# Kernel optimization log

Measured on AMD Instinct MI355X. Metric: run time of the kernel, lower is better.

## Reference

```python
import jax, jax.numpy as jnp
import numpy as np

D_EEG = 256; D_QUERY = 256; D_MODEL = 256; NUM_HEADS = 8
D_HEAD = D_MODEL // NUM_HEADS; PROJ_DIM = 40
B = 32; N = 4096


def _rope(x):
    # x: (B, S, H, D) -- rotate along sequence dim with interleaved-pair convention
    S, D = x.shape[1], x.shape[-1]
    inv = 1.0 / (10000.0 ** (jnp.arange(0, D, 2, dtype=jnp.float32) / D))
    f = jnp.arange(S, dtype=jnp.float32)[:, None] * inv[None, :]        # (S, D/2)
    cos = jnp.repeat(jnp.cos(f), 2, axis=-1)[None, :, None, :]
    sin = jnp.repeat(jnp.sin(f), 2, axis=-1)[None, :, None, :]
    xp = x.reshape(x.shape[:-1] + (D // 2, 2))
    rot = jnp.stack([-xp[..., 1], xp[..., 0]], axis=-1).reshape(x.shape)
    return x * cos + rot * sin


def _ln(x, g, b):
    m = x.mean(-1, keepdims=True)
    v = x.var(-1, keepdims=True)
    return (x - m) / jnp.sqrt(v + 1e-5) * g + b


def _l2norm(x):
    return x / jnp.maximum(jnp.linalg.norm(x, axis=-1, keepdims=True), 1e-12)


def setup_inputs():
    key = jax.random.key(0)
    ks = jax.random.split(key, 16)

    def lin(k, din, dout):
        s = 1.0 / np.sqrt(din)
        w = jax.random.uniform(k, (din, dout), minval=-s, maxval=s, dtype=jnp.float32)
        b = jax.random.uniform(jax.random.fold_in(k, 1), (dout,), minval=-s, maxval=s, dtype=jnp.float32)
        return w, b

    eeg_w, eeg_b = lin(ks[0], D_EEG, D_MODEL)
    stim_w, stim_b = lin(ks[1], D_QUERY, D_MODEL)
    temp_w, temp_b = lin(ks[2], D_QUERY, D_MODEL)
    q_w, q_b = lin(ks[3], D_MODEL, D_MODEL)
    k_w, k_b = lin(ks[4], D_MODEL, D_MODEL)
    v_w, v_b = lin(ks[5], D_MODEL, D_MODEL)
    fc_w, fc_b = lin(ks[6], D_MODEL, PROJ_DIM)

    return {
        "eeg_feat": jax.random.normal(ks[7], (B, N, D_EEG), dtype=jnp.float32),
        "stim_feat": jax.random.normal(ks[8], (B, D_QUERY), dtype=jnp.float32),
        "temp_feat": jax.random.normal(ks[9], (B, D_QUERY), dtype=jnp.float32),
        "eeg_w": eeg_w, "eeg_b": eeg_b,
        "stim_w": stim_w, "stim_b": stim_b,
        "temp_w": temp_w, "temp_b": temp_b,
        "q_w": q_w, "q_b": q_b,
        "k_w": k_w, "k_b": k_b,
        "v_w": v_w, "v_b": v_b,
        "fc_w": fc_w, "fc_b": fc_b,
        "lnq_g": jnp.ones((D_MODEL,), jnp.float32), "lnq_b": jnp.zeros((D_MODEL,), jnp.float32),
        "lnk_g": jnp.ones((D_MODEL,), jnp.float32), "lnk_b": jnp.zeros((D_MODEL,), jnp.float32),
    }


def reference(eeg_feat, stim_feat, temp_feat, eeg_w, eeg_b, stim_w, stim_b,
              temp_w, temp_b, q_w, q_b, k_w, k_b, v_w, v_b, fc_w, fc_b,
              lnq_g, lnq_b, lnk_g, lnk_b):
    Bq = eeg_feat.shape[0]
    eeg = eeg_feat @ eeg_w + eeg_b                      # (B, N, D)
    stim = (stim_feat @ stim_w + stim_b)[:, None, :]
    temp = (temp_feat @ temp_w + temp_b)[:, None, :]
    query = jnp.concatenate([stim, temp], axis=1)        # (B, 2, D)

    query = _ln(query, lnq_g, lnq_b)
    kv = _ln(eeg, lnk_g, lnk_b)

    Q = (query @ q_w + q_b).reshape(Bq, 2, NUM_HEADS, D_HEAD)
    K = (kv @ k_w + k_b).reshape(Bq, -1, NUM_HEADS, D_HEAD)
    V = (kv @ v_w + v_b).reshape(Bq, -1, NUM_HEADS, D_HEAD)

    Q = _l2norm(_rope(Q))
    K = _l2norm(_rope(K))

    scores = jnp.einsum('bqhd,bkhd->bhqk', Q, K) / np.sqrt(D_HEAD)
    scale = jax.lax.stop_gradient(
        jnp.maximum(jnp.std(scores, axis=-1, ddof=1, keepdims=True), 1e-3))
    scores = jnp.tanh(scores / (2.0 * scale)) * (5.0 * scale)

    w = jax.nn.softmax(scores, axis=-1)
    w = (w + 1e-4) / (w.sum(-1, keepdims=True) + 1e-8)

    attn_out = jnp.einsum('bhqk,bkhd->bqhd', w, V).reshape(Bq, 2, D_MODEL)
    pooled = attn_out.mean(axis=1)
    logits = pooled @ fc_w + fc_b
    return logits, pooled, attn_out, query
```

## Files before the change

### kernel.cpp

```cpp
#include <hip/hip_runtime.h>
#include <hip/hip_bf16.h>
#include <math.h>

#define TID ((int)threadIdx.x)

typedef float f32x4 __attribute__((ext_vector_type(4)));
typedef short s16x8 __attribute__((ext_vector_type(8)));

__device__ __forceinline__ unsigned short f2bf(float f) {
  union { float f; unsigned u; } v; v.f = f;
  unsigned r = v.u + 0x7FFFu + ((v.u >> 16) & 1u);
  return (unsigned short)(r >> 16);
}
__device__ __forceinline__ float bf2f(unsigned short h) {
  union { unsigned u; float f; } v; v.u = ((unsigned)h) << 16;
  return v.f;
}

__global__ void prep_kernel(const float* __restrict__ eeg_w,
                            const float* __restrict__ k_w,
                            const float* __restrict__ v_w,
                            unsigned short* __restrict__ wt,
                            float2* __restrict__ trig) {
  int gid = blockIdx.x * 256 + TID;
  if (gid < 3 * 65536) {
    int m = gid >> 16, e = gid & 65535;
    int i = e >> 8, j = e & 255;
    const float* W = (m == 0) ? eeg_w : ((m == 1) ? k_w : v_w);
    wt[m * 65536 + j * 256 + i] = f2bf(W[i * 256 + j]);
  } else {
    int e = gid - 3 * 65536;
    int n = e >> 4, p = e & 15;
    float inv = exp2f(-(float)p * 0.8304820237218406f);
    float a = (float)n * inv;
    trig[e] = make_float2(cosf(a), sinf(a));
  }
}

__global__ __launch_bounds__(256) void q_kernel(
    const float* __restrict__ stim_feat, const float* __restrict__ temp_feat,
    const float* __restrict__ stim_w, const float* __restrict__ stim_b,
    const float* __restrict__ temp_w, const float* __restrict__ temp_b,
    const float* __restrict__ q_w, const float* __restrict__ q_b,
    const float* __restrict__ lnq_g, const float* __restrict__ lnq_b,
    float* __restrict__ out_query, float* __restrict__ qhat) {
  int b = blockIdx.x >> 1, q = blockIdx.x & 1;
  __shared__ float f[256];
  __shared__ float red[8];
  const float* feat = (q ? temp_feat : stim_feat) + b * 256;
  const float* W = q ? temp_w : stim_w;
  const float* bias = q ? temp_b : stim_b;
  f[TID] = feat[TID];
  __syncthreads();
  float acc = bias[TID];
#pragma unroll 8
  for (int i = 0; i < 256; ++i) acc = fmaf(f[i], W[i * 256 + TID], acc);
  float s1 = acc, s2 = acc * acc;
#pragma unroll
  for (int m = 1; m < 64; m <<= 1) { s1 += __shfl_xor(s1, m, 64); s2 += __shfl_xor(s2, m, 64); }
  if ((TID & 63) == 0) { red[TID >> 6] = s1; red[4 + (TID >> 6)] = s2; }
  __syncthreads();
  s1 = red[0] + red[1] + red[2] + red[3];
  s2 = red[4] + red[5] + red[6] + red[7];
  float mean = s1 * (1.f / 256.f);
  float var = s2 * (1.f / 256.f) - mean * mean;
  float rstd = rsqrtf(var + 1e-5f);
  float qln = (acc - mean) * rstd * lnq_g[TID] + lnq_b[TID];
  out_query[(b * 2 + q) * 256 + TID] = qln;
  __syncthreads();
  f[TID] = qln;
  __syncthreads();
  float a2 = q_b[TID];
#pragma unroll 8
  for (int i = 0; i < 256; ++i) a2 = fmaf(f[i], q_w[i * 256 + TID], a2);
  __syncthreads();
  f[TID] = a2;
  __syncthreads();
  float partner = f[TID ^ 1];
  int p = (TID >> 1) & 15;
  float inv = exp2f(-(float)p * 0.8304820237218406f);
  float ang = (float)q * inv;
  float cc_ = cosf(ang), ss_ = sinf(ang);
  float r = (TID & 1) ? fmaf(a2, cc_, partner * ss_) : fmaf(a2, cc_, -partner * ss_);
  float sq = r * r;
#pragma unroll
  for (int m = 1; m < 32; m <<= 1) sq += __shfl_xor(sq, m, 32);
  float rs = 1.f / fmaxf(sqrtf(sq), 1e-12f);
  qhat[(b * 2 + q) * 256 + TID] = r * rs;
}

__global__ __launch_bounds__(256) void main_kernel(
    const float* __restrict__ x,
    const float* __restrict__ eeg_b,
    const float* __restrict__ k_b,
    const float* __restrict__ v_b,
    const float* __restrict__ lnk_g,
    const float* __restrict__ lnk_b,
    const unsigned short* __restrict__ wt_eeg,
    const unsigned short* __restrict__ wt_k,
    const unsigned short* __restrict__ wt_v,
    const float2* __restrict__ trig,
    const float* __restrict__ qhat,
    float* __restrict__ scores,
    unsigned short* __restrict__ vws) {

  __shared__ __align__(16) unsigned short A[64 * 256];
  __shared__ __align__(16) unsigned short K2[64 * 256];
  __shared__ __align__(16) float TRQH[2048];
  __shared__ float2 ST[64];

  float* PS = (float*)K2;
  float2* TR = (float2*)TRQH;

  const int tid = TID;
  const int w = tid >> 6, l = tid & 63, g = l >> 4, c = l & 15;
  const int r0 = blockIdx.x * 64;
  const int b = r0 >> 12;
  const int n0 = r0 & 4095;

#pragma unroll
  for (int i = 0; i < 8; ++i) {
    int ch = i * 256 + tid;
    int row = ch >> 5, cc = ch & 31;
    const float4* gp = (const float4*)(x + (size_t)(r0 + row) * 256 + cc * 8);
    float4 u0 = gp[0], u1 = gp[1];
    s16x8 pk;
    pk[0] = (short)f2bf(u0.x); pk[1] = (short)f2bf(u0.y);
    pk[2] = (short)f2bf(u0.z); pk[3] = (short)f2bf(u0.w);
    pk[4] = (short)f2bf(u1.x); pk[5] = (short)f2bf(u1.y);
    pk[6] = (short)f2bf(u1.z); pk[7] = (short)f2bf(u1.w);
    *(s16x8*)&A[row * 256 + ((cc ^ (row & 7)) * 8)] = pk;
  }
#pragma unroll
  for (int i = 0; i < 4; ++i) {
    int e = i * 256 + tid;
    int rr = e >> 4, pp = e & 15;
    TR[e] = trig[(size_t)(n0 + rr) * 16 + pp];
  }
  __syncthreads();

  f32x4 acc[4][4];

#define DO_GEMM(WT) do {                                                          \
    _Pragma("unroll") for (int rb = 0; rb < 4; ++rb)                              \
      _Pragma("unroll") for (int cb = 0; cb < 4; ++cb)                            \
        acc[rb][cb] = (f32x4){0.f, 0.f, 0.f, 0.f};                                \
    _Pragma("unroll") for (int ks = 0; ks < 8; ++ks) {                            \
      s16x8 af[4]; s16x8 bfr[4];                                                  \
      _Pragma("unroll") for (int rb = 0; rb < 4; ++rb) {                          \
        int row = rb * 16 + c; int kc = ks * 4 + g;                               \
        af[rb] = *(const s16x8*)&A[row * 256 + ((kc ^ (row & 7)) * 8)];           \
      }                                                                           \
      _Pragma("unroll") for (int cb = 0; cb < 4; ++cb) {                          \
        int col = w * 64 + cb * 16 + c;                                           \
        bfr[cb] = *(const s16x8*)&(WT)[col * 256 + ks * 32 + g * 8];              \
      }                                                                           \
      _Pragma("unroll") for (int rb = 0; rb < 4; ++rb)                            \
        _Pragma("unroll") for (int cb = 0; cb < 4; ++cb)                          \
          acc[rb][cb] = __builtin_amdgcn_mfma_f32_16x16x32_bf16(                  \
              af[rb], bfr[cb], acc[rb][cb], 0, 0, 0);                             \
    } } while (0)

  float ebias[4], kbias[4], vbias[4], gg[4], bb[4];
  int cols[4];
#pragma unroll
  for (int cb = 0; cb < 4; ++cb) {
    int col = w * 64 + cb * 16 + c;
    cols[cb] = col;
    ebias[cb] = eeg_b[col]; kbias[cb] = k_b[col]; vbias[cb] = v_b[col];
    gg[cb] = lnk_g[col]; bb[cb] = lnk_b[col];
  }

  DO_GEMM(wt_eeg);

  {
    float ps[4][4], pq[4][4];
#pragma unroll
    for (int rb = 0; rb < 4; ++rb)
#pragma unroll
      for (int r = 0; r < 4; ++r) {
        float s = 0.f, q2 = 0.f;
#pragma unroll
        for (int cb = 0; cb < 4; ++cb) {
          float v = acc[rb][cb][r] + ebias[cb];
          s += v; q2 += v * v;
        }
        ps[rb][r] = s; pq[rb][r] = q2;
      }
#pragma unroll
    for (int m = 1; m < 16; m <<= 1)
#pragma unroll
      for (int rb = 0; rb < 4; ++rb)
#pragma unroll
        for (int r = 0; r < 4; ++r) {
          ps[rb][r] += __shfl_xor(ps[rb][r], m, 64);
          pq[rb][r] += __shfl_xor(pq[rb][r], m, 64);
        }
    float outS = 0.f, outQ = 0.f;
#pragma unroll
    for (int rb = 0; rb < 4; ++rb)
#pragma unroll
      for (int r = 0; r < 4; ++r)
        if (c == rb * 4 + r) { outS = ps[rb][r]; outQ = pq[rb][r]; }
    int row = (c >> 2) * 16 + g * 4 + (c & 3);
    PS[row * 8 + w * 2 + 0] = outS;
    PS[row * 8 + w * 2 + 1] = outQ;
  }
  __syncthreads();
  if (tid < 64) {
    float s = PS[tid * 8 + 0] + PS[tid * 8 + 2] + PS[tid * 8 + 4] + PS[tid * 8 + 6];
    float q2 = PS[tid * 8 + 1] + PS[tid * 8 + 3] + PS[tid * 8 + 5] + PS[tid * 8 + 7];
    float mean = s * (1.f / 256.f);
    float var = q2 * (1.f / 256.f) - mean * mean;
    ST[tid] = make_float2(mean, rsqrtf(var + 1e-5f));
  }
  __syncthreads();

#pragma unroll
  for (int rb = 0; rb < 4; ++rb)
#pragma unroll
    for (int r = 0; r < 4; ++r) {
      int row = rb * 16 + g * 4 + r;
      float2 st = ST[row];
#pragma unroll
      for (int cb = 0; cb < 4; ++cb) {
        float v = (acc[rb][cb][r] + ebias[cb] - st.x) * st.y * gg[cb] + bb[cb];
        A[row * 256 + (cols[cb] ^ ((row & 7) * 8))] = f2bf(v);
      }
    }
  __syncthreads();

  DO_GEMM(wt_k);
#pragma unroll
  for (int rb = 0; rb < 4; ++rb)
#pragma unroll
    for (int cb = 0; cb < 4; ++cb) {
      int pp = (cols[cb] >> 1) & 15;
#pragma unroll
      for (int r = 0; r < 4; ++r) {
        int row = rb * 16 + g * 4 + r;
        float v = acc[rb][cb][r] + kbias[cb];
        float pv = __shfl_xor(v, 1, 64);
        float2 cs2 = TR[row * 16 + pp];
        float rv = (c & 1) ? fmaf(v, cs2.x, pv * cs2.y)
                           : fmaf(v, cs2.x, -pv * cs2.y);
        K2[row * 256 + (cols[cb] ^ ((row & 7) * 8))] = f2bf(rv);
      }
    }

  DO_GEMM(wt_v);
  __syncthreads();

#pragma unroll
  for (int rb = 0; rb < 4; ++rb)
#pragma unroll
    for (int r = 0; r < 4; ++r) {
      int row = rb * 16 + g * 4 + r;
#pragma unroll
      for (int cb = 0; cb < 4; ++cb)
        A[row * 256 + cols[cb]] = f2bf(acc[rb][cb][r] + vbias[cb]);
    }
  TRQH[tid] = qhat[(size_t)b * 512 + tid];
  TRQH[256 + tid] = qhat[(size_t)b * 512 + 256 + tid];
  __syncthreads();

#pragma unroll
  for (int i = 0; i < 2; ++i) {
    int hr = i * 256 + tid;
    int row = hr >> 3, hh = hr & 7;
    const s16x8* src = (const s16x8*)&A[row * 256 + hh * 32];
    s16x8 v0 = src[0], v1 = src[1], v2 = src[2], v3 = src[3];
    s16x8* dst = (s16x8*)&vws[((size_t)(b * 8 + hh) * 4096 + n0 + row) * 32];
    dst[0] = v0; dst[1] = v1; dst[2] = v2; dst[3] = v3;
  }

#pragma unroll
  for (int cell = 0; cell < 2; ++cell) {
    int h = cell * 4 + w;
    int row = l;
    float ssq = 0.f, d0 = 0.f, d1 = 0.f;
#pragma unroll
    for (int j = 0; j < 4; ++j) {
      s16x8 kv = *(const s16x8*)&K2[row * 256 + (((h * 4 + j) ^ (row & 7)) * 8)];
#pragma unroll
      for (int t = 0; t < 8; ++t) {
        float kf = bf2f((unsigned short)kv[t]);
        int col = h * 32 + j * 8 + t;
        ssq = fmaf(kf, kf, ssq);
        d0 = fmaf(kf, TRQH[col], d0);
        d1 = fmaf(kf, TRQH[256 + col], d1);
      }
    }
    float is = 0.17677669529663687f / fmaxf(sqrtf(ssq), 1e-12f);
    scores[(size_t)((b * 8 + h) * 2 + 0) * 4096 + n0 + row] = d0 * is;
    scores[(size_t)((b * 8 + h) * 2 + 1) * 4096 + n0 + row] = d1 * is;
  }
#undef DO_GEMM
}

__global__ __launch_bounds__(256) void attn_kernel(
    const float* __restrict__ scores,
    const unsigned short* __restrict__ vws,
    float* __restrict__ out_attn) {
  int b = blockIdx.x >> 3, h = blockIdx.x & 7;
  const float* s0p = scores + (size_t)((b * 8 + h) * 2 + 0) * 4096;
  const float* s1p = scores + (size_t)((b * 8 + h) * 2 + 1) * 4096;
  float sa[16], sb[16];
  float a1 = 0.f, a2 = 0.f, b1 = 0.f, b2 = 0.f;
#pragma unroll
  for (int i = 0; i < 16; ++i) {
    int k = i * 256 + TID;
    sa[i] = s0p[k]; sb[i] = s1p[k];
    a1 += sa[i]; a2 += sa[i] * sa[i];
    b1 += sb[i]; b2 += sb[i] * sb[i];
  }
  __shared__ float red[16];
  int w = TID >> 6;
#pragma unroll
  for (int m = 1; m < 64; m <<= 1) {
    a1 += __shfl_xor(a1, m, 64); a2 += __shfl_xor(a2, m, 64);
    b1 += __shfl_xor(b1, m, 64); b2 += __shfl_xor(b2, m, 64);
  }
  if ((TID & 63) == 0) { red[w * 4] = a1; red[w * 4 + 1] = a2; red[w * 4 + 2] = b1; red[w * 4 + 3] = b2; }
  __syncthreads();
  a1 = red[0] + red[4] + red[8] + red[12];
  a2 = red[1] + red[5] + red[9] + red[13];
  b1 = red[2] + red[6] + red[10] + red[14];
  b2 = red[3] + red[7] + red[11] + red[15];
  float va = (a2 - a1 * a1 * (1.f / 4096.f)) * (1.f / 4095.f);
  float vb = (b2 - b1 * b1 * (1.f / 4096.f)) * (1.f / 4095.f);
  float sga = fmaxf(sqrtf(fmaxf(va, 0.f)), 1e-3f);
  float sgb = fmaxf(sqrtf(fmaxf(vb, 0.f)), 1e-3f);
  float ia = 0.5f / sga, ib = 0.5f / sgb;
  float fa = 5.f * sga, fb = 5.f * sgb;
  float ea = 0.f, eb = 0.f;
#pragma unroll
  for (int i = 0; i < 16; ++i) {
    sa[i] = __expf(tanhf(sa[i] * ia) * fa);
    sb[i] = __expf(tanhf(sb[i] * ib) * fb);
    ea += sa[i]; eb += sb[i];
  }
#pragma unroll
  for (int m = 1; m < 64; m <<= 1) { ea += __shfl_xor(ea, m, 64); eb += __shfl_xor(eb, m, 64); }
  __syncthreads();
  if ((TID & 63) == 0) { red[w * 2] = ea; red[w * 2 + 1] = eb; }
  __syncthreads();
  ea = red[0] + red[2] + red[4] + red[6];
  eb = red[1] + red[3] + red[5] + red[7];
  float iea = 1.f / ea, ieb = 1.f / eb;
  float oa[32], ob[32];
#pragma unroll
  for (int d = 0; d < 32; ++d) { oa[d] = 0.f; ob[d] = 0.f; }
  const unsigned short* vbase = vws + (size_t)(b * 8 + h) * 4096 * 32;
#pragma unroll 4
  for (int i = 0; i < 16; ++i) {
    int k = i * 256 + TID;
    float wa = fmaf(sa[i], iea, 1e-4f);
    float wb = fmaf(sb[i], ieb, 1e-4f);
    const s16x8* vp = (const s16x8*)(vbase + (size_t)k * 32);
#pragma unroll
    for (int j = 0; j < 4; ++j) {
      s16x8 vv = vp[j];
#pragma unroll
      for (int t = 0; t < 8; ++t) {
        float vf = bf2f((unsigned short)vv[t]);
        oa[j * 8 + t] = fmaf(wa, vf, oa[j * 8 + t]);
        ob[j * 8 + t] = fmaf(wb, vf, ob[j * 8 + t]);
      }
    }
  }
#pragma unroll
  for (int m = 1; m < 64; m <<= 1) {
#pragma unroll
    for (int d = 0; d < 32; ++d) { oa[d] += __shfl_xor(oa[d], m, 64); ob[d] += __shfl_xor(ob[d], m, 64); }
  }
  __shared__ float R[4][64];
  if ((TID & 63) == 0) {
#pragma unroll
    for (int d = 0; d < 32; ++d) { R[w][d] = oa[d]; R[w][32 + d] = ob[d]; }
  }
  __syncthreads();
  if (TID < 64) {
    float s = R[0][TID] + R[1][TID] + R[2][TID] + R[3][TID];
    int q = TID >> 5, d = TID & 31;
    out_attn[(b * 2 + q) * 256 + h * 32 + d] = s;
  }
}

__global__ __launch_bounds__(256) void final_kernel(
    const float* __restrict__ attn, const float* __restrict__ fc_w,
    const float* __restrict__ fc_b, float* __restrict__ out_pooled,
    float* __restrict__ out_logits) {
  int b = blockIdx.x;
  __shared__ float P[256];
  float p = 0.5f * (attn[(b * 2) * 256 + TID] + attn[(b * 2 + 1) * 256 + TID]);
  out_pooled[b * 256 + TID] = p;
  P[TID] = p;
  __syncthreads();
  if (TID < 40) {
    float acc = fc_b[TID];
#pragma unroll 8
    for (int i = 0; i < 256; ++i) acc = fmaf(P[i], fc_w[i * 40 + TID], acc);
    out_logits[b * 40 + TID] = acc;
  }
}

extern "C" void kernel_launch(void* const* d_in, const int* in_sizes, int n_in,
                              void* d_out, int out_size, void* d_ws, size_t ws_size,
                              hipStream_t stream) {
  (void)in_sizes; (void)n_in; (void)out_size; (void)ws_size;
  const float* eeg_feat  = (const float*)d_in[0];
  const float* stim_feat = (const float*)d_in[1];
  const float* temp_feat = (const float*)d_in[2];
  const float* eeg_w = (const float*)d_in[3];
  const float* eeg_b = (const float*)d_in[4];
  const float* stim_w = (const float*)d_in[5];
  const float* stim_b = (const float*)d_in[6];
  const float* temp_w = (const float*)d_in[7];
  const float* temp_b = (const float*)d_in[8];
  const float* q_w = (const float*)d_in[9];
  const float* q_b = (const float*)d_in[10];
  const float* k_w = (const float*)d_in[11];
  const float* k_b = (const float*)d_in[12];
  const float* v_w = (const float*)d_in[13];
  const float* v_b = (const float*)d_in[14];
  const float* fc_w = (const float*)d_in[15];
  const float* fc_b = (const float*)d_in[16];
  const float* lnq_g = (const float*)d_in[17];
  const float* lnq_b = (const float*)d_in[18];
  const float* lnk_g = (const float*)d_in[19];
  const float* lnk_b = (const float*)d_in[20];

  char* ws = (char*)d_ws;
  unsigned short* wt  = (unsigned short*)(ws + 0);
  float2* trig        = (float2*)(ws + 393216);
  float* qhat         = (float*)(ws + 917504);
  float* scores       = (float*)(ws + 1048576);
  unsigned short* vws = (unsigned short*)(ws + 9437184);

  float* out = (float*)d_out;
  float* out_logits = out;
  float* out_pooled = out + 1280;
  float* out_attn   = out + 9472;
  float* out_query  = out + 25856;

  prep_kernel<<<1024, 256, 0, stream>>>(eeg_w, k_w, v_w, wt, trig);
  q_kernel<<<64, 256, 0, stream>>>(stim_feat, temp_feat, stim_w, stim_b,
                                   temp_w, temp_b, q_w, q_b, lnq_g, lnq_b,
                                   out_query, qhat);
  main_kernel<<<2048, 256, 0, stream>>>(eeg_feat, eeg_b, k_b, v_b, lnk_g, lnk_b,
                                        wt, wt + 65536, wt + 131072,
                                        trig, qhat, scores, vws);
  attn_kernel<<<256, 256, 0, stream>>>(scores, vws, out_attn);
  final_kernel<<<32, 256, 0, stream>>>(out_attn, fc_w, fc_b, out_pooled, out_logits);
}
```

Measured before the change: 255.5 us.

## Split fused main kernel into LN-projection and K/V kernels with register-cached weights

The single fused kernel is split into two. The first does the eeg projection and LayerNorm, preloads the weight fragments into registers, and writes the normalized bf16 activations to a workspace buffer. The second uses 512-thread blocks where half the waves compute K and half compute V concurrently, loops over four 64-row tiles per block, and prefetches the next tile from global memory into registers. This aims to reduce register pressure and raise occupancy and parallelism, at the cost of an extra 64 MB bf16 round trip through global memory and an additional kernel launch.

```diff
diff --git a/kernel.cpp b/kernel.cpp
--- a/kernel.cpp
+++ b/kernel.cpp
@@ -16,6 +16,9 @@
   union { unsigned u; float f; } v; v.u = ((unsigned)h) << 16;
   return v.f;
 }
+
+#define BAR_LGKM() do { asm volatile("s_waitcnt lgkmcnt(0)" ::: "memory"); \
+                        __builtin_amdgcn_s_barrier(); } while (0)
 
 __global__ void prep_kernel(const float* __restrict__ eeg_w,
                             const float* __restrict__ k_w,
@@ -89,34 +92,28 @@
   qhat[(b * 2 + q) * 256 + TID] = r * rs;
 }
 
-__global__ __launch_bounds__(256) void main_kernel(
+__global__ __launch_bounds__(256, 2) void eeg_ln_kernel(
     const float* __restrict__ x,
     const float* __restrict__ eeg_b,
-    const float* __restrict__ k_b,
-    const float* __restrict__ v_b,
     const float* __restrict__ lnk_g,
     const float* __restrict__ lnk_b,
     const unsigned short* __restrict__ wt_eeg,
-    const unsigned short* __restrict__ wt_k,
-    const unsigned short* __restrict__ wt_v,
-    const float2* __restrict__ trig,
-    const float* __restrict__ qhat,
-    float* __restrict__ scores,
-    unsigned short* __restrict__ vws) {
+    unsigned short* __restrict__ xp) {
 
   __shared__ __align__(16) unsigned short A[64 * 256];
-  __shared__ __align__(16) unsigned short K2[64 * 256];
-  __shared__ __align__(16) float TRQH[2048];
+  __shared__ float PS[64 * 8];
   __shared__ float2 ST[64];
-
-  float* PS = (float*)K2;
-  float2* TR = (float2*)TRQH;
 
   const int tid = TID;
   const int w = tid >> 6, l = tid & 63, g = l >> 4, c = l & 15;
   const int r0 = blockIdx.x * 64;
-  const int b = r0 >> 12;
-  const int n0 = r0 & 4095;
+
+  s16x8 bA[8][2];
+#pragma unroll
+  for (int ks = 0; ks < 8; ++ks)
+#pragma unroll
+    for (int j = 0; j < 2; ++j)
+      bA[ks][j] = *(const s16x8*)&wt_eeg[(size_t)(w * 64 + j * 16 + c) * 256 + ks * 32 + g * 8];
 
 #pragma unroll
   for (int i = 0; i < 8; ++i) {
@@ -131,47 +128,57 @@
     pk[6] = (short)f2bf(u1.z); pk[7] = (short)f2bf(u1.w);
     *(s16x8*)&A[row * 256 + ((cc ^ (row & 7)) * 8)] = pk;
   }
-#pragma unroll
-  for (int i = 0; i < 4; ++i) {
-    int e = i * 256 + tid;
-    int rr = e >> 4, pp = e & 15;
-    TR[e] = trig[(size_t)(n0 + rr) * 16 + pp];
-  }
-  __syncthreads();
-
-  f32x4 acc[4][4];
-
-#define DO_GEMM(WT) do {                                                          \
-    _Pragma("unroll") for (int rb = 0; rb < 4; ++rb)                              \
-      _Pragma("unroll") for (int cb = 0; cb < 4; ++cb)                            \
-        acc[rb][cb] = (f32x4){0.f, 0.f, 0.f, 0.f};                                \
-    _Pragma("unroll") for (int ks = 0; ks < 8; ++ks) {                            \
-      s16x8 af[4]; s16x8 bfr[4];                                                  \
-      _Pragma("unroll") for (int rb = 0; rb < 4; ++rb) {                          \
-        int row = rb * 16 + c; int kc = ks * 4 + g;                               \
-        af[rb] = *(const s16x8*)&A[row * 256 + ((kc ^ (row & 7)) * 8)];           \
-      }                                                                           \
-      _Pragma("unroll") for (int cb = 0; cb < 4; ++cb) {                          \
-        int col = w * 64 + cb * 16 + c;                                           \
-        bfr[cb] = *(const s16x8*)&(WT)[col * 256 + ks * 32 + g * 8];              \
-      }                                                                           \
-      _Pragma("unroll") for (int rb = 0; rb < 4; ++rb)                            \
-        _Pragma("unroll") for (int cb = 0; cb < 4; ++cb)                          \
-          acc[rb][cb] = __builtin_amdgcn_mfma_f32_16x16x32_bf16(                  \
-              af[rb], bfr[cb], acc[rb][cb], 0, 0, 0);                             \
-    } } while (0)
-
-  float ebias[4], kbias[4], vbias[4], gg[4], bb[4];
+
+  float ebias[4], gg[4], bb[4];
   int cols[4];
 #pragma unroll
   for (int cb = 0; cb < 4; ++cb) {
     int col = w * 64 + cb * 16 + c;
     cols[cb] = col;
-    ebias[cb] = eeg_b[col]; kbias[cb] = k_b[col]; vbias[cb] = v_b[col];
-    gg[cb] = lnk_g[col]; bb[cb] = lnk_b[col];
-  }
-
-  DO_GEMM(wt_eeg);
+    ebias[cb] = eeg_b[col]; gg[cb] = lnk_g[col]; bb[cb] = lnk_b[col];
+  }
+  __syncthreads();
+
+  f32x4 acc[4][4];
+#pragma unroll
+  for (int rb = 0; rb < 4; ++rb)
+#pragma unroll
+    for (int cb = 0; cb < 4; ++cb) acc[rb][cb] = (f32x4){0.f, 0.f, 0.f, 0.f};
+
+#pragma unroll
+  for (int ks = 0; ks < 8; ++ks) {
+    s16x8 af[4];
+#pragma unroll
+    for (int rb = 0; rb < 4; ++rb) {
+      int row = rb * 16 + c; int kc = ks * 4 + g;
+      af[rb] = *(const s16x8*)&A[row * 256 + ((kc ^ (row & 7)) * 8)];
+    }
+#pragma unroll
+    for (int rb = 0; rb < 4; ++rb)
+#pragma unroll
+      for (int j = 0; j < 2; ++j)
+        acc[rb][j] = __builtin_amdgcn_mfma_f32_16x16x32_bf16(af[rb], bA[ks][j], acc[rb][j], 0, 0, 0);
+  }
+  s16x8 bB[8][2];
+#pragma unroll
+  for (int ks = 0; ks < 8; ++ks)
+#pragma unroll
+    for (int j = 0; j < 2; ++j)
+      bB[ks][j] = *(const s16x8*)&wt_eeg[(size_t)(w * 64 + (2 + j) * 16 + c) * 256 + ks * 32 + g * 8];
+#pragma unroll
+  for (int ks = 0; ks < 8; ++ks) {
+    s16x8 af[4];
+#pragma unroll
+    for (int rb = 0; rb < 4; ++rb) {
+      int row = rb * 16 + c; int kc = ks * 4 + g;
+      af[rb] = *(const s16x8*)&A[row * 256 + ((kc ^ (row & 7)) * 8)];
+    }
+#pragma unroll
+    for (int rb = 0; rb < 4; ++rb)
+#pragma unroll
+      for (int j = 0; j < 2; ++j)
+        acc[rb][2 + j] = __builtin_amdgcn_mfma_f32_16x16x32_bf16(af[rb], bB[ks][j], acc[rb][2 + j], 0, 0, 0);
+  }
 
   {
     float ps[4][4], pq[4][4];
@@ -230,72 +237,166 @@
     }
   __syncthreads();
 
-  DO_GEMM(wt_k);
-#pragma unroll
-  for (int rb = 0; rb < 4; ++rb)
-#pragma unroll
-    for (int cb = 0; cb < 4; ++cb) {
-      int pp = (cols[cb] >> 1) & 15;
-#pragma unroll
-      for (int r = 0; r < 4; ++r) {
-        int row = rb * 16 + g * 4 + r;
-        float v = acc[rb][cb][r] + kbias[cb];
-        float pv = __shfl_xor(v, 1, 64);
-        float2 cs2 = TR[row * 16 + pp];
-        float rv = (c & 1) ? fmaf(v, cs2.x, pv * cs2.y)
-                           : fmaf(v, cs2.x, -pv * cs2.y);
-        K2[row * 256 + (cols[cb] ^ ((row & 7) * 8))] = f2bf(rv);
+#pragma unroll
+  for (int j = 0; j < 8; ++j) {
+    int gidx = tid + 256 * j;
+    *(s16x8*)&xp[(size_t)r0 * 256 + (size_t)gidx * 8] = *(const s16x8*)&A[gidx * 8];
+  }
+}
+
+__global__ __launch_bounds__(512, 2) void kv_kernel(
+    const unsigned short* __restrict__ xp,
+    const float* __restrict__ k_b,
+    const float* __restrict__ v_b,
+    const unsigned short* __restrict__ wt_k,
+    const unsigned short* __restrict__ wt_v,
+    const float2* __restrict__ trig,
+    const float* __restrict__ qhat,
+    float* __restrict__ scores,
+    unsigned short* __restrict__ vws) {
+
+  __shared__ __align__(16) unsigned short A[64 * 256];
+  __shared__ __align__(16) unsigned short K2[64 * 256];
+  __shared__ __align__(16) float2 TR[1024];
+  __shared__ float QH[512];
+
+  const int tid = TID;
+  const int w8 = tid >> 6, l = tid & 63, g = l >> 4, c = l & 15;
+  const int kv = w8 >> 2;
+  const int w = w8 & 3;
+  const int blkrow0 = blockIdx.x * 256;
+  const int b = blkrow0 >> 12;
+
+  const unsigned short* wsel = kv ? wt_v : wt_k;
+  const float* bsel = kv ? v_b : k_b;
+
+  float bias[4];
+  int cols[4];
+#pragma unroll
+  for (int cb = 0; cb < 4; ++cb) {
+    int col = w * 64 + cb * 16 + c;
+    cols[cb] = col;
+    bias[cb] = bsel[col];
+  }
+
+  QH[tid] = qhat[(size_t)b * 512 + tid];
+  s16x8 pf0, pf1, pf2, pf3;
+  float2 ptr0, ptr1;
+  {
+    const s16x8* src = (const s16x8*)&xp[(size_t)blkrow0 * 256];
+    pf0 = src[tid]; pf1 = src[tid + 512]; pf2 = src[tid + 1024]; pf3 = src[tid + 1536];
+    int e0 = tid, e1 = tid + 512;
+    ptr0 = trig[(size_t)((blkrow0 & 4095) + (e0 >> 4)) * 16 + (e0 & 15)];
+    ptr1 = trig[(size_t)((blkrow0 & 4095) + (e1 >> 4)) * 16 + (e1 & 15)];
+  }
+
+  for (int t = 0; t < 4; ++t) {
+    const int row0 = blkrow0 + t * 64;
+    const int n0 = row0 & 4095;
+
+    BAR_LGKM();
+    {
+      s16x8* dst = (s16x8*)A;
+      dst[tid] = pf0; dst[tid + 512] = pf1; dst[tid + 1024] = pf2; dst[tid + 1536] = pf3;
+      TR[tid] = ptr0; TR[tid + 512] = ptr1;
+    }
+    BAR_LGKM();
+
+    if (t < 3) {
+      const s16x8* src = (const s16x8*)&xp[(size_t)(row0 + 64) * 256];
+      pf0 = src[tid]; pf1 = src[tid + 512]; pf2 = src[tid + 1024]; pf3 = src[tid + 1536];
+      int e0 = tid, e1 = tid + 512;
+      ptr0 = trig[(size_t)((n0 + 64) + (e0 >> 4)) * 16 + (e0 & 15)];
+      ptr1 = trig[(size_t)((n0 + 64) + (e1 >> 4)) * 16 + (e1 & 15)];
+    }
+
+    f32x4 acc[4][4];
+#pragma unroll
+    for (int rb = 0; rb < 4; ++rb)
+#pragma unroll
+      for (int cb = 0; cb < 4; ++cb) acc[rb][cb] = (f32x4){0.f, 0.f, 0.f, 0.f};
+#pragma unroll
+    for (int h = 0; h < 2; ++h) {
+      s16x8 bfr[8][2];
+#pragma unroll
+      for (int ks = 0; ks < 8; ++ks)
+#pragma unroll
+        for (int j = 0; j < 2; ++j)
+          bfr[ks][j] = *(const s16x8*)&wsel[(size_t)(w * 64 + (h * 2 + j) * 16 + c) * 256 + ks * 32 + g * 8];
+#pragma unroll
+      for (int ks = 0; ks < 8; ++ks) {
+        s16x8 af[4];
+#pragma unroll
+        for (int rb = 0; rb < 4; ++rb) {
+          int row = rb * 16 + c; int kc = ks * 4 + g;
+          af[rb] = *(const s16x8*)&A[row * 256 + ((kc ^ (row & 7)) * 8)];
+        }
+#pragma unroll
+        for (int rb = 0; rb < 4; ++rb)
+#pragma unroll
+          for (int j = 0; j < 2; ++j)
+            acc[rb][h * 2 + j] = __builtin_amdgcn_mfma_f32_16x16x32_bf16(af[rb], bfr[ks][j], acc[rb][h * 2 + j], 0, 0, 0);
       }
     }
-
-  DO_GEMM(wt_v);
-  __syncthreads();
-
-#pragma unroll
-  for (int rb = 0; rb < 4; ++rb)
-#pragma unroll
-    for (int r = 0; r < 4; ++r) {
-      int row = rb * 16 + g * 4 + r;
-#pragma unroll
-      for (int cb = 0; cb < 4; ++cb)
-        A[row * 256 + cols[cb]] = f2bf(acc[rb][cb][r] + vbias[cb]);
-    }
-  TRQH[tid] = qhat[(size_t)b * 512 + tid];
-  TRQH[256 + tid] = qhat[(size_t)b * 512 + 256 + tid];
-  __syncthreads();
-
-#pragma unroll
-  for (int i = 0; i < 2; ++i) {
-    int hr = i * 256 + tid;
-    int row = hr >> 3, hh = hr & 7;
-    const s16x8* src = (const s16x8*)&A[row * 256 + hh * 32];
-    s16x8 v0 = src[0], v1 = src[1], v2 = src[2], v3 = src[3];
-    s16x8* dst = (s16x8*)&vws[((size_t)(b * 8 + hh) * 4096 + n0 + row) * 32];
-    dst[0] = v0; dst[1] = v1; dst[2] = v2; dst[3] = v3;
-  }
-
-#pragma unroll
-  for (int cell = 0; cell < 2; ++cell) {
-    int h = cell * 4 + w;
-    int row = l;
-    float ssq = 0.f, d0 = 0.f, d1 = 0.f;
-#pragma unroll
-    for (int j = 0; j < 4; ++j) {
-      s16x8 kv = *(const s16x8*)&K2[row * 256 + (((h * 4 + j) ^ (row & 7)) * 8)];
-#pragma unroll
-      for (int t = 0; t < 8; ++t) {
-        float kf = bf2f((unsigned short)kv[t]);
-        int col = h * 32 + j * 8 + t;
-        ssq = fmaf(kf, kf, ssq);
-        d0 = fmaf(kf, TRQH[col], d0);
-        d1 = fmaf(kf, TRQH[256 + col], d1);
+    BAR_LGKM();
+
+    if (kv == 0) {
+#pragma unroll
+      for (int rb = 0; rb < 4; ++rb)
+#pragma unroll
+        for (int cb = 0; cb < 4; ++cb) {
+          int pp = (cols[cb] >> 1) & 15;
+#pragma unroll
+          for (int r = 0; r < 4; ++r) {
+            int row = rb * 16 + g * 4 + r;
+            float v = acc[rb][cb][r] + bias[cb];
+            float pv = __shfl_xor(v, 1, 64);
+            float2 cs2 = TR[row * 16 + pp];
+            float rv = (c & 1) ? fmaf(v, cs2.x, pv * cs2.y)
+                               : fmaf(v, cs2.x, -pv * cs2.y);
+            K2[row * 256 + (cols[cb] ^ ((row & 7) * 8))] = f2bf(rv);
+          }
+        }
+    } else {
+#pragma unroll
+      for (int rb = 0; rb < 4; ++rb)
+#pragma unroll
+        for (int r = 0; r < 4; ++r) {
+          int row = rb * 16 + g * 4 + r;
+#pragma unroll
+          for (int cb = 0; cb < 4; ++cb)
+            A[row * 256 + cols[cb]] = f2bf(acc[rb][cb][r] + bias[cb]);
+        }
+    }
+    BAR_LGKM();
+
+    {
+      int row = tid >> 3, hh = tid & 7;
+      const s16x8* src = (const s16x8*)&A[row * 256 + hh * 32];
+      s16x8 v0 = src[0], v1 = src[1], v2 = src[2], v3 = src[3];
+      s16x8* dst = (s16x8*)&vws[((size_t)(b * 8 + hh) * 4096 + n0 + row) * 32];
+      dst[0] = v0; dst[1] = v1; dst[2] = v2; dst[3] = v3;
+    }
+    {
+      int h = w8, row = l;
+      float ssq = 0.f, d0 = 0.f, d1 = 0.f;
+#pragma unroll
+      for (int j = 0; j < 4; ++j) {
+        s16x8 kvv = *(const s16x8*)&K2[row * 256 + (((h * 4 + j) ^ (row & 7)) * 8)];
+#pragma unroll
+        for (int t8 = 0; t8 < 8; ++t8) {
+          float kf = bf2f((unsigned short)kvv[t8]);
+          int col = h * 32 + j * 8 + t8;
+          ssq = fmaf(kf, kf, ssq);
+          d0 = fmaf(kf, QH[col], d0);
+          d1 = fmaf(kf, QH[256 + col], d1);
+        }
       }
-    }
-    float is = 0.17677669529663687f / fmaxf(sqrtf(ssq), 1e-12f);
-    scores[(size_t)((b * 8 + h) * 2 + 0) * 4096 + n0 + row] = d0 * is;
-    scores[(size_t)((b * 8 + h) * 2 + 1) * 4096 + n0 + row] = d1 * is;
-  }
-#undef DO_GEMM
+      float is = 0.17677669529663687f / fmaxf(sqrtf(ssq), 1e-12f);
+      scores[(size_t)((b * 8 + h) * 2 + 0) * 4096 + n0 + row] = d0 * is;
+      scores[(size_t)((b * 8 + h) * 2 + 1) * 4096 + n0 + row] = d1 * is;
+    }
+  }
 }
 
 __global__ __launch_bounds__(256) void attn_kernel(
@@ -436,7 +537,8 @@
   float2* trig        = (float2*)(ws + 393216);
   float* qhat         = (float*)(ws + 917504);
   float* scores       = (float*)(ws + 1048576);
-  unsigned short* vws = (unsigned short*)(ws + 9437184);
+  unsigned short* xp  = (unsigned short*)(ws + 9437184);
+  unsigned short* vws = (unsigned short*)(ws + 76546048);
 
   float* out = (float*)d_out;
   float* out_logits = out;
@@ -448,9 +550,9 @@
   q_kernel<<<64, 256, 0, stream>>>(stim_feat, temp_feat, stim_w, stim_b,
                                    temp_w, temp_b, q_w, q_b, lnq_g, lnq_b,
                                    out_query, qhat);
-  main_kernel<<<2048, 256, 0, stream>>>(eeg_feat, eeg_b, k_b, v_b, lnk_g, lnk_b,
-                                        wt, wt + 65536, wt + 131072,
-                                        trig, qhat, scores, vws);
+  eeg_ln_kernel<<<2048, 256, 0, stream>>>(eeg_feat, eeg_b, lnk_g, lnk_b, wt, xp);
+  kv_kernel<<<512, 512, 0, stream>>>(xp, k_b, v_b, wt + 65536, wt + 131072,
+                                     trig, qhat, scores, vws);
   attn_kernel<<<256, 256, 0, stream>>>(scores, vws, out_attn);
   final_kernel<<<32, 256, 0, stream>>>(out_attn, fc_w, fc_b, out_pooled, out_logits);
 }
```

Result: slower. 438.2 us (+71.5%).

## Defer V projection by pooling normalized activations per head before applying v_w

Applied to the files above, without the earlier changes.

The per-token V GEMM is removed from the main kernel. The LayerNorm-normalized activations are written out in bf16, attention weights are materialized, and a new ysum kernel forms per-head weighted sums of those activations. A finish kernel then applies v_w and a scaled v_b once per (batch, head, query), using the fact that the renormalized weights sum to a constant. Dropping the K2 LDS buffer and the V GEMM cuts compute and shared memory, and the kernel now requests 3 blocks per CU. RoPE is applied on the fly from global trig. In exchange there is an extra scores-to-weights pass and a partial-sum buffer, and the bias factor 1.4096 is hard-coded to N=4096.

```diff
diff --git a/kernel.cpp b/kernel.cpp
--- a/kernel.cpp
+++ b/kernel.cpp
@@ -19,17 +19,16 @@
 
 __global__ void prep_kernel(const float* __restrict__ eeg_w,
                             const float* __restrict__ k_w,
-                            const float* __restrict__ v_w,
                             unsigned short* __restrict__ wt,
                             float2* __restrict__ trig) {
   int gid = blockIdx.x * 256 + TID;
-  if (gid < 3 * 65536) {
+  if (gid < 2 * 65536) {
     int m = gid >> 16, e = gid & 65535;
     int i = e >> 8, j = e & 255;
-    const float* W = (m == 0) ? eeg_w : ((m == 1) ? k_w : v_w);
+    const float* W = (m == 0) ? eeg_w : k_w;
     wt[m * 65536 + j * 256 + i] = f2bf(W[i * 256 + j]);
   } else {
-    int e = gid - 3 * 65536;
+    int e = gid - 2 * 65536;
     int n = e >> 4, p = e & 15;
     float inv = exp2f(-(float)p * 0.8304820237218406f);
     float a = (float)n * inv;
@@ -89,28 +88,24 @@
   qhat[(b * 2 + q) * 256 + TID] = r * rs;
 }
 
-__global__ __launch_bounds__(256) void main_kernel(
+__global__ __launch_bounds__(256, 3) void main_kernel(
     const float* __restrict__ x,
     const float* __restrict__ eeg_b,
     const float* __restrict__ k_b,
-    const float* __restrict__ v_b,
     const float* __restrict__ lnk_g,
     const float* __restrict__ lnk_b,
     const unsigned short* __restrict__ wt_eeg,
     const unsigned short* __restrict__ wt_k,
-    const unsigned short* __restrict__ wt_v,
     const float2* __restrict__ trig,
     const float* __restrict__ qhat,
     float* __restrict__ scores,
-    unsigned short* __restrict__ vws) {
+    unsigned short* __restrict__ xp) {
 
   __shared__ __align__(16) unsigned short A[64 * 256];
-  __shared__ __align__(16) unsigned short K2[64 * 256];
-  __shared__ __align__(16) float TRQH[2048];
+  __shared__ float PS[64 * 9];
   __shared__ float2 ST[64];
 
-  float* PS = (float*)K2;
-  float2* TR = (float2*)TRQH;
+  float* QH = PS;
 
   const int tid = TID;
   const int w = tid >> 6, l = tid & 63, g = l >> 4, c = l & 15;
@@ -130,12 +125,6 @@
     pk[4] = (short)f2bf(u1.x); pk[5] = (short)f2bf(u1.y);
     pk[6] = (short)f2bf(u1.z); pk[7] = (short)f2bf(u1.w);
     *(s16x8*)&A[row * 256 + ((cc ^ (row & 7)) * 8)] = pk;
-  }
-#pragma unroll
-  for (int i = 0; i < 4; ++i) {
-    int e = i * 256 + tid;
-    int rr = e >> 4, pp = e & 15;
-    TR[e] = trig[(size_t)(n0 + rr) * 16 + pp];
   }
   __syncthreads();
 
@@ -161,13 +150,13 @@
               af[rb], bfr[cb], acc[rb][cb], 0, 0, 0);                             \
     } } while (0)
 
-  float ebias[4], kbias[4], vbias[4], gg[4], bb[4];
+  float ebias[4], kbias[4], gg[4], bb[4];
   int cols[4];
 #pragma unroll
   for (int cb = 0; cb < 4; ++cb) {
     int col = w * 64 + cb * 16 + c;
     cols[cb] = col;
-    ebias[cb] = eeg_b[col]; kbias[cb] = k_b[col]; vbias[cb] = v_b[col];
+    ebias[cb] = eeg_b[col]; kbias[cb] = k_b[col];
     gg[cb] = lnk_g[col]; bb[cb] = lnk_b[col];
   }
 
@@ -203,19 +192,21 @@
       for (int r = 0; r < 4; ++r)
         if (c == rb * 4 + r) { outS = ps[rb][r]; outQ = pq[rb][r]; }
     int row = (c >> 2) * 16 + g * 4 + (c & 3);
-    PS[row * 8 + w * 2 + 0] = outS;
-    PS[row * 8 + w * 2 + 1] = outQ;
+    PS[row * 9 + w * 2 + 0] = outS;
+    PS[row * 9 + w * 2 + 1] = outQ;
   }
   __syncthreads();
   if (tid < 64) {
-    float s = PS[tid * 8 + 0] + PS[tid * 8 + 2] + PS[tid * 8 + 4] + PS[tid * 8 + 6];
-    float q2 = PS[tid * 8 + 1] + PS[tid * 8 + 3] + PS[tid * 8 + 5] + PS[tid * 8 + 7];
+    float s = PS[tid * 9 + 0] + PS[tid * 9 + 2] + PS[tid * 9 + 4] + PS[tid * 9 + 6];
+    float q2 = PS[tid * 9 + 1] + PS[tid * 9 + 3] + PS[tid * 9 + 5] + PS[tid * 9 + 7];
     float mean = s * (1.f / 256.f);
     float var = q2 * (1.f / 256.f) - mean * mean;
     ST[tid] = make_float2(mean, rsqrtf(var + 1e-5f));
   }
   __syncthreads();
 
+  QH[tid] = qhat[(size_t)b * 512 + tid];
+  QH[256 + tid] = qhat[(size_t)b * 512 + 256 + tid];
 #pragma unroll
   for (int rb = 0; rb < 4; ++rb)
 #pragma unroll
@@ -230,25 +221,15 @@
     }
   __syncthreads();
 
+#pragma unroll
+  for (int i = 0; i < 8; ++i) {
+    int e = i * 256 + tid;
+    int row = e >> 5, u = e & 31;
+    s16x8 v = *(const s16x8*)&A[row * 256 + ((u ^ (row & 7)) * 8)];
+    *(s16x8*)&xp[(size_t)(r0 + row) * 256 + u * 8] = v;
+  }
+
   DO_GEMM(wt_k);
-#pragma unroll
-  for (int rb = 0; rb < 4; ++rb)
-#pragma unroll
-    for (int cb = 0; cb < 4; ++cb) {
-      int pp = (cols[cb] >> 1) & 15;
-#pragma unroll
-      for (int r = 0; r < 4; ++r) {
-        int row = rb * 16 + g * 4 + r;
-        float v = acc[rb][cb][r] + kbias[cb];
-        float pv = __shfl_xor(v, 1, 64);
-        float2 cs2 = TR[row * 16 + pp];
-        float rv = (c & 1) ? fmaf(v, cs2.x, pv * cs2.y)
-                           : fmaf(v, cs2.x, -pv * cs2.y);
-        K2[row * 256 + (cols[cb] ^ ((row & 7) * 8))] = f2bf(rv);
-      }
-    }
-
-  DO_GEMM(wt_v);
   __syncthreads();
 
 #pragma unroll
@@ -258,37 +239,33 @@
       int row = rb * 16 + g * 4 + r;
 #pragma unroll
       for (int cb = 0; cb < 4; ++cb)
-        A[row * 256 + cols[cb]] = f2bf(acc[rb][cb][r] + vbias[cb]);
+        A[row * 256 + (cols[cb] ^ ((row & 7) * 8))] = f2bf(acc[rb][cb][r] + kbias[cb]);
     }
-  TRQH[tid] = qhat[(size_t)b * 512 + tid];
-  TRQH[256 + tid] = qhat[(size_t)b * 512 + 256 + tid];
-  __syncthreads();
-
-#pragma unroll
-  for (int i = 0; i < 2; ++i) {
-    int hr = i * 256 + tid;
-    int row = hr >> 3, hh = hr & 7;
-    const s16x8* src = (const s16x8*)&A[row * 256 + hh * 32];
-    s16x8 v0 = src[0], v1 = src[1], v2 = src[2], v3 = src[3];
-    s16x8* dst = (s16x8*)&vws[((size_t)(b * 8 + hh) * 4096 + n0 + row) * 32];
-    dst[0] = v0; dst[1] = v1; dst[2] = v2; dst[3] = v3;
-  }
+  __syncthreads();
 
 #pragma unroll
   for (int cell = 0; cell < 2; ++cell) {
     int h = cell * 4 + w;
     int row = l;
+    const float2* tgp = trig + (size_t)(n0 + row) * 16;
+    float2 tg[16];
+#pragma unroll
+    for (int i = 0; i < 16; ++i) tg[i] = tgp[i];
     float ssq = 0.f, d0 = 0.f, d1 = 0.f;
 #pragma unroll
     for (int j = 0; j < 4; ++j) {
-      s16x8 kv = *(const s16x8*)&K2[row * 256 + (((h * 4 + j) ^ (row & 7)) * 8)];
-#pragma unroll
-      for (int t = 0; t < 8; ++t) {
-        float kf = bf2f((unsigned short)kv[t]);
-        int col = h * 32 + j * 8 + t;
-        ssq = fmaf(kf, kf, ssq);
-        d0 = fmaf(kf, TRQH[col], d0);
-        d1 = fmaf(kf, TRQH[256 + col], d1);
+      s16x8 kvv = *(const s16x8*)&A[row * 256 + (((h * 4 + j) ^ (row & 7)) * 8)];
+#pragma unroll
+      for (int t = 0; t < 4; ++t) {
+        float e0 = bf2f((unsigned short)kvv[2 * t]);
+        float e1 = bf2f((unsigned short)kvv[2 * t + 1]);
+        float2 cs = tg[j * 4 + t];
+        float rv0 = e0 * cs.x - e1 * cs.y;
+        float rv1 = fmaf(e1, cs.x, e0 * cs.y);
+        int col = h * 32 + j * 8 + 2 * t;
+        ssq = fmaf(rv0, rv0, fmaf(rv1, rv1, ssq));
+        d0 = fmaf(rv0, QH[col], fmaf(rv1, QH[col + 1], d0));
+        d1 = fmaf(rv0, QH[256 + col], fmaf(rv1, QH[256 + col + 1], d1));
       }
     }
     float is = 0.17677669529663687f / fmaxf(sqrtf(ssq), 1e-12f);
@@ -298,10 +275,8 @@
 #undef DO_GEMM
 }
 
-__global__ __launch_bounds__(256) void attn_kernel(
-    const float* __restrict__ scores,
-    const unsigned short* __restrict__ vws,
-    float* __restrict__ out_attn) {
+__global__ __launch_bounds__(256) void wgt_kernel(
+    const float* __restrict__ scores, float* __restrict__ wbuf) {
   int b = blockIdx.x >> 3, h = blockIdx.x & 7;
   const float* s0p = scores + (size_t)((b * 8 + h) * 2 + 0) * 4096;
   const float* s1p = scores + (size_t)((b * 8 + h) * 2 + 1) * 4096;
@@ -348,52 +323,76 @@
   ea = red[0] + red[2] + red[4] + red[6];
   eb = red[1] + red[3] + red[5] + red[7];
   float iea = 1.f / ea, ieb = 1.f / eb;
-  float oa[32], ob[32];
-#pragma unroll
-  for (int d = 0; d < 32; ++d) { oa[d] = 0.f; ob[d] = 0.f; }
-  const unsigned short* vbase = vws + (size_t)(b * 8 + h) * 4096 * 32;
-#pragma unroll 4
+  float* w0 = wbuf + ((size_t)(b * 16) + h * 2 + 0) * 4096;
+  float* w1 = w0 + 4096;
+#pragma unroll
   for (int i = 0; i < 16; ++i) {
     int k = i * 256 + TID;
-    float wa = fmaf(sa[i], iea, 1e-4f);
-    float wb = fmaf(sb[i], ieb, 1e-4f);
-    const s16x8* vp = (const s16x8*)(vbase + (size_t)k * 32);
-#pragma unroll
-    for (int j = 0; j < 4; ++j) {
-      s16x8 vv = vp[j];
-#pragma unroll
-      for (int t = 0; t < 8; ++t) {
-        float vf = bf2f((unsigned short)vv[t]);
-        oa[j * 8 + t] = fmaf(wa, vf, oa[j * 8 + t]);
-        ob[j * 8 + t] = fmaf(wb, vf, ob[j * 8 + t]);
-      }
+    w0[k] = fmaf(sa[i], iea, 1e-4f);
+    w1[k] = fmaf(sb[i], ieb, 1e-4f);
+  }
+}
+
+__global__ __launch_bounds__(256) void ysum_kernel(
+    const unsigned short* __restrict__ xp, const float* __restrict__ wbuf,
+    float* __restrict__ ypart) {
+  int b = blockIdx.x >> 5, slab = blockIdx.x & 31;
+  int h = TID >> 5, cg = TID & 31;
+  const unsigned short* xb = xp + ((size_t)b * 4096 + slab * 128) * 256 + cg * 8;
+  const float* w0 = wbuf + ((size_t)(b * 16) + h * 2 + 0) * 4096 + slab * 128;
+  const float* w1 = w0 + 4096;
+  float y0[8], y1[8];
+#pragma unroll
+  for (int t = 0; t < 8; ++t) { y0[t] = 0.f; y1[t] = 0.f; }
+#pragma unroll 4
+  for (int r = 0; r < 128; ++r) {
+    s16x8 xv = *(const s16x8*)(xb + (size_t)r * 256);
+    float wa = w0[r], wc = w1[r];
+#pragma unroll
+    for (int t = 0; t < 8; ++t) {
+      float xf = bf2f((unsigned short)xv[t]);
+      y0[t] = fmaf(wa, xf, y0[t]);
+      y1[t] = fmaf(wc, xf, y1[t]);
     }
   }
-#pragma unroll
-  for (int m = 1; m < 64; m <<= 1) {
-#pragma unroll
-    for (int d = 0; d < 32; ++d) { oa[d] += __shfl_xor(oa[d], m, 64); ob[d] += __shfl_xor(ob[d], m, 64); }
-  }
-  __shared__ float R[4][64];
-  if ((TID & 63) == 0) {
-#pragma unroll
-    for (int d = 0; d < 32; ++d) { R[w][d] = oa[d]; R[w][32 + d] = ob[d]; }
-  }
-  __syncthreads();
-  if (TID < 64) {
-    float s = R[0][TID] + R[1][TID] + R[2][TID] + R[3][TID];
-    int q = TID >> 5, d = TID & 31;
-    out_attn[(b * 2 + q) * 256 + h * 32 + d] = s;
-  }
-}
-
-__global__ __launch_bounds__(256) void final_kernel(
-    const float* __restrict__ attn, const float* __restrict__ fc_w,
-    const float* __restrict__ fc_b, float* __restrict__ out_pooled,
-    float* __restrict__ out_logits) {
+  float* yp = ypart + (((size_t)(b * 32 + slab) * 16) + h * 2) * 256 + cg * 8;
+  *(float4*)&yp[0] = (float4){y0[0], y0[1], y0[2], y0[3]};
+  *(float4*)&yp[4] = (float4){y0[4], y0[5], y0[6], y0[7]};
+  *(float4*)&yp[256] = (float4){y1[0], y1[1], y1[2], y1[3]};
+  *(float4*)&yp[260] = (float4){y1[4], y1[5], y1[6], y1[7]};
+}
+
+__global__ __launch_bounds__(256) void finish_kernel(
+    const float* __restrict__ ypart, const float* __restrict__ v_w,
+    const float* __restrict__ v_b, const float* __restrict__ fc_w,
+    const float* __restrict__ fc_b, float* __restrict__ out_attn,
+    float* __restrict__ out_pooled, float* __restrict__ out_logits) {
   int b = blockIdx.x;
+  __shared__ float Y[16][256];
+  __shared__ float ATT[2][256];
   __shared__ float P[256];
-  float p = 0.5f * (attn[(b * 2) * 256 + TID] + attn[(b * 2 + 1) * 256 + TID]);
+  for (int idx = TID; idx < 4096; idx += 256) {
+    int hq = idx >> 8, cc = idx & 255;
+    float s = 0.f;
+#pragma unroll 8
+    for (int sl = 0; sl < 32; ++sl)
+      s += ypart[(((size_t)(b * 32 + sl) * 16) + hq) * 256 + cc];
+    Y[hq][cc] = s;
+  }
+  __syncthreads();
+#pragma unroll
+  for (int o = TID; o < 512; o += 256) {
+    int q = o >> 8, dout = o & 255;
+    int hq = (dout >> 5) * 2 + q;
+    float acc = 1.4096f * v_b[dout];
+#pragma unroll 8
+    for (int c2 = 0; c2 < 256; ++c2)
+      acc = fmaf(Y[hq][c2], v_w[c2 * 256 + dout], acc);
+    out_attn[(b * 2 + q) * 256 + dout] = acc;
+    ATT[q][dout] = acc;
+  }
+  __syncthreads();
+  float p = 0.5f * (ATT[0][TID] + ATT[1][TID]);
   out_pooled[b * 256 + TID] = p;
   P[TID] = p;
   __syncthreads();
@@ -436,7 +435,9 @@
   float2* trig        = (float2*)(ws + 393216);
   float* qhat         = (float*)(ws + 917504);
   float* scores       = (float*)(ws + 1048576);
-  unsigned short* vws = (unsigned short*)(ws + 9437184);
+  float* wbuf         = (float*)(ws + 9437184);
+  unsigned short* xp  = (unsigned short*)(ws + 17825792);
+  float* ypart        = (float*)(ws + 84934656);
 
   float* out = (float*)d_out;
   float* out_logits = out;
@@ -444,13 +445,14 @@
   float* out_attn   = out + 9472;
   float* out_query  = out + 25856;
 
-  prep_kernel<<<1024, 256, 0, stream>>>(eeg_w, k_w, v_w, wt, trig);
+  prep_kernel<<<768, 256, 0, stream>>>(eeg_w, k_w, wt, trig);
   q_kernel<<<64, 256, 0, stream>>>(stim_feat, temp_feat, stim_w, stim_b,
                                    temp_w, temp_b, q_w, q_b, lnq_g, lnq_b,
                                    out_query, qhat);
-  main_kernel<<<2048, 256, 0, stream>>>(eeg_feat, eeg_b, k_b, v_b, lnk_g, lnk_b,
-                                        wt, wt + 65536, wt + 131072,
-                                        trig, qhat, scores, vws);
-  attn_kernel<<<256, 256, 0, stream>>>(scores, vws, out_attn);
-  final_kernel<<<32, 256, 0, stream>>>(out_attn, fc_w, fc_b, out_pooled, out_logits);
-}
+  main_kernel<<<2048, 256, 0, stream>>>(eeg_feat, eeg_b, k_b, lnk_g, lnk_b,
+                                        wt, wt + 65536, trig, qhat, scores, xp);
+  wgt_kernel<<<256, 256, 0, stream>>>(scores, wbuf);
+  ysum_kernel<<<1024, 256, 0, stream>>>(xp, wbuf, ypart);
+  finish_kernel<<<32, 256, 0, stream>>>(ypart, v_w, v_b, fc_w, fc_b,
+                                        out_attn, out_pooled, out_logits);
+}
```

Result: slower. 283.3 us (+10.9%).
